# Performance work log

Measured on AMD Instinct MI355X. Metric: run time of the kernel, lower is better.

The kernel has to match this reference:

```python
import jax, jax.numpy as jnp
from jax import lax
import numpy as np

D_MODEL = 768
D_STATE = 64
D_CONV = 4
EXPAND = 2
D_INNER = EXPAND * D_MODEL          # 1536
HEADDIM = 64
H = D_INNER // HEADDIM              # 24 heads
CONV_DIM = D_INNER + 2 * D_STATE    # 1664 (x, B, C share the conv)
D_IN_PROJ = 2 * D_INNER + 2 * D_STATE + H  # z, xBC, dt
BATCH, SEQ = 4, 4096


def _mamba2(x, in_w, conv_w, conv_b, dt_bias, A_log, Dp, norm_w, out_w):
    """Mamba2 forward (ngroups=1, no in/out-proj bias), faithful to mamba_ssm reference path."""
    Bb, L, _ = x.shape
    zxbcdt = x @ in_w.T                                   # (B,L,D_IN_PROJ)
    z = zxbcdt[..., :D_INNER]
    xBC = zxbcdt[..., D_INNER:D_INNER + CONV_DIM]
    dt = zxbcdt[..., D_INNER + CONV_DIM:]                 # (B,L,H)
    # causal depthwise conv1d over time + SiLU
    xBC = xBC.transpose(0, 2, 1)                          # (B,C,L)
    xBC = lax.conv_general_dilated(xBC, conv_w, (1,), [(D_CONV - 1, 0)],
                                   feature_group_count=CONV_DIM,
                                   dimension_numbers=('NCH', 'OIH', 'NCH'))
    xBC = jax.nn.silu(xBC + conv_b[None, :, None]).transpose(0, 2, 1)
    xs = xBC[..., :D_INNER].reshape(Bb, L, H, HEADDIM)    # (B,L,H,P)
    Bc = xBC[..., D_INNER:D_INNER + D_STATE]              # (B,L,N)
    Cc = xBC[..., D_INNER + D_STATE:]                     # (B,L,N)
    dt = jax.nn.softplus(dt + dt_bias)                    # (B,L,H)
    dA = jnp.exp(dt * (-jnp.exp(A_log)))                  # (B,L,H)
    dtx = dt[..., None] * xs                              # (B,L,H,P)

    def step(h, inp):
        dA_t, dtx_t, B_t, C_t = inp
        h = h * dA_t[:, :, None, None] + jnp.einsum('bhp,bn->bhpn', dtx_t, B_t)
        y = jnp.einsum('bhpn,bn->bhp', h, C_t)
        return h, y

    h0 = jnp.zeros((Bb, H, HEADDIM, D_STATE), x.dtype)
    _, ys = lax.scan(step, h0, (jnp.moveaxis(dA, 1, 0), jnp.moveaxis(dtx, 1, 0),
                                jnp.moveaxis(Bc, 1, 0), jnp.moveaxis(Cc, 1, 0)))
    y = jnp.moveaxis(ys, 0, 1) + Dp[None, None, :, None] * xs  # skip term D*x
    y = y.reshape(Bb, L, D_INNER)
    # RMSNormGated (norm_before_gate=False): gate then normalize
    y = y * jax.nn.silu(z)
    y = y * lax.rsqrt(jnp.mean(y * y, -1, keepdims=True) + 1e-5) * norm_w
    return y @ out_w.T                                    # (B,L,D_MODEL)


def _mamba_params(key, scale=0.02):
    ks = jax.random.split(key, 5)
    in_w = jax.random.normal(ks[0], (D_IN_PROJ, D_MODEL), jnp.float32) * scale
    conv_w = jax.random.normal(ks[1], (CONV_DIM, 1, D_CONV), jnp.float32) * 0.2
    conv_b = jnp.zeros((CONV_DIM,), jnp.float32)
    dt = jax.random.uniform(ks[2], (H,), jnp.float32, 0.001, 0.1)
    dt_bias = dt + jnp.log(-jnp.expm1(-dt))               # inverse softplus
    A_log = jnp.log(jax.random.uniform(ks[3], (H,), jnp.float32, 1.0, 16.0))
    Dp = jnp.ones((H,), jnp.float32)
    norm_w = jnp.ones((D_INNER,), jnp.float32)
    out_w = jax.random.normal(ks[4], (D_MODEL, D_INNER), jnp.float32) * scale
    return in_w, conv_w, conv_b, dt_bias, A_log, Dp, norm_w, out_w


def setup_inputs() -> dict:
    key = jax.random.key(0)
    kx, kf, kb, kw = jax.random.split(key, 4)
    x = jax.random.normal(kx, (BATCH, SEQ, D_MODEL), jnp.float32)
    f = _mamba_params(kf)
    b = _mamba_params(kb)
    fus_w = jax.random.normal(kw, (D_MODEL, 2 * D_MODEL), jnp.float32) * 0.02
    fus_b = jnp.zeros((D_MODEL,), jnp.float32)
    names = ['in_w', 'conv_w', 'conv_b', 'dt_bias', 'A_log', 'D', 'norm_w', 'out_w']
    inp = {'x': x, 'fus_w': fus_w, 'fus_b': fus_b}
    for n, v in zip(names, f):
        inp['f_' + n] = v
    for n, v in zip(names, b):
        inp['b_' + n] = v
    return inp


def reference(x, fus_w, fus_b,
              f_in_w, f_conv_w, f_conv_b, f_dt_bias, f_A_log, f_D, f_norm_w, f_out_w,
              b_in_w, b_conv_w, b_conv_b, b_dt_bias, b_A_log, b_D, b_norm_w, b_out_w):
    out_f = _mamba2(x, f_in_w, f_conv_w, f_conv_b, f_dt_bias, f_A_log, f_D, f_norm_w, f_out_w)
    out_b = jnp.flip(_mamba2(jnp.flip(x, 1), b_in_w, b_conv_w, b_conv_b,
                             b_dt_bias, b_A_log, b_D, b_norm_w, b_out_w), 1)
    out = jnp.concatenate([out_f, out_b], axis=-1)        # (B,L,2*D_MODEL)
    return out @ fus_w.T + fus_b
```

## Files before the change

kernel.cpp:

```cpp
#include <hip/hip_runtime.h>
#include <hip/hip_bf16.h>


#define BATCHN 4
#define SEQL 4096
#define DMODEL 768
#define DINNER 1536
#define DSTATE 64
#define HN 24
#define CONVDIM 1664
#define NROWS_XBC 3200
#define NTOK (BATCHN*SEQL)
#define NCHUNK 64
#define LS 72

typedef short v8s __attribute__((ext_vector_type(8)));
typedef unsigned short v8u __attribute__((ext_vector_type(8)));
typedef float v4f __attribute__((ext_vector_type(4)));
typedef unsigned int v2u32 __attribute__((ext_vector_type(2)));
typedef __hip_bfloat16 bf16;

__device__ __forceinline__ int flip_row(int r) {
  return (r & ~4095) | (4095 - (r & 4095));
}
__device__ __forceinline__ float us2f(unsigned short u) {
  return __uint_as_float(((unsigned int)u) << 16);
}
__device__ __forceinline__ unsigned short f2us(float f) {
  bf16 b = __float2bfloat16(f);
  return __builtin_bit_cast(unsigned short, b);
}
__device__ __forceinline__ void async16(const unsigned short* g, unsigned short* l) {
  __builtin_amdgcn_global_load_lds(
      (const __attribute__((address_space(1))) unsigned int*)(const void*)g,
      (__attribute__((address_space(3))) unsigned int*)(void*)l, 16, 0, 0);
}


__global__ void cast_x_kernel(const float* __restrict__ x, bf16* __restrict__ xf) {
  int idx = blockIdx.x * 256 + threadIdx.x;
  v4f v = *(const v4f*)(x + (size_t)idx * 4);
  v2u32 o;
  o[0] = (unsigned int)f2us(v[0]) | ((unsigned int)f2us(v[1]) << 16);
  o[1] = (unsigned int)f2us(v[2]) | ((unsigned int)f2us(v[3]) << 16);
  *(v2u32*)((unsigned short*)xf + (size_t)idx * 4) = o;
}

__global__ void cast_kernel(const float* __restrict__ src, bf16* __restrict__ dst) {
  int idx = blockIdx.x * 256 + threadIdx.x;
  v4f v = *(const v4f*)(src + (size_t)idx * 4);
  v2u32 o;
  o[0] = (unsigned int)f2us(v[0]) | ((unsigned int)f2us(v[1]) << 16);
  o[1] = (unsigned int)f2us(v[2]) | ((unsigned int)f2us(v[3]) << 16);
  *(v2u32*)((unsigned short*)dst + (size_t)idx * 4) = o;
}

__global__ void cast_strided_kernel(const float* __restrict__ src, bf16* __restrict__ dst,
                                    int cols, int src_stride) {
  int idx4 = (blockIdx.x * 256 + threadIdx.x) * 4;
  int j = idx4 / cols, m = idx4 % cols;
  v4f v = *(const v4f*)(src + (size_t)j * src_stride + m);
  v2u32 o;
  o[0] = (unsigned int)f2us(v[0]) | ((unsigned int)f2us(v[1]) << 16);
  o[1] = (unsigned int)f2us(v[2]) | ((unsigned int)f2us(v[3]) << 16);
  *(v2u32*)((unsigned short*)dst + idx4) = o;
}

__global__ void transpose_ow_kernel(const float* __restrict__ src, bf16* __restrict__ dst) {
  int idx4 = (blockIdx.x * 256 + threadIdx.x) * 4;
  int k = idx4 / DMODEL, c0 = idx4 % DMODEL;
  unsigned short u[4];
#pragma unroll
  for (int i = 0; i < 4; i++)
    u[i] = f2us(src[(size_t)(c0 + i) * DINNER + k]);
  v2u32 o;
  o[0] = (unsigned int)u[0] | ((unsigned int)u[1] << 16);
  o[1] = (unsigned int)u[2] | ((unsigned int)u[3] << 16);
  *(v2u32*)((unsigned short*)dst + idx4) = o;
}

template <bool OUT_BF16>
__global__ __launch_bounds__(256) void gemm_lds(
    const bf16* __restrict__ A, const bf16* __restrict__ B, void* __restrict__ C,
    int K, int ldc, int flip_a, int flip_c, int accum, const float* __restrict__ bias) {
  __shared__ unsigned short sA[128 * 32];
  __shared__ unsigned short sB[128 * 32];
  int tid = threadIdx.x;
  int wave = tid >> 6, lane = tid & 63;
  int l15 = lane & 15, quad = lane >> 4;
  int m0 = blockIdx.x * 128, n0 = blockIdx.y * 128;
  int mw = (wave >> 1) * 64, nw = (wave & 1) * 64;

  int srow = wave * 32 + (lane >> 2);
  int scol = (lane & 3) * 8;
  const unsigned short* Ap = (const unsigned short*)A;
  const unsigned short* Bp = (const unsigned short*)B;
  int ar0 = m0 + srow, ar1 = m0 + srow + 16;
  if (flip_a) { ar0 = flip_row(ar0); ar1 = flip_row(ar1); }
  const unsigned short* ga0 = Ap + (size_t)ar0 * K + scol;
  const unsigned short* ga1 = Ap + (size_t)ar1 * K + scol;
  const unsigned short* gb0 = Bp + (size_t)(n0 + srow) * K + scol;
  const unsigned short* gb1 = Bp + (size_t)(n0 + srow + 16) * K + scol;
  unsigned short* lA0 = &sA[(wave * 32) * 32];
  unsigned short* lA1 = &sA[(wave * 32 + 16) * 32];
  unsigned short* lB0 = &sB[(wave * 32) * 32];
  unsigned short* lB1 = &sB[(wave * 32 + 16) * 32];

  v4f acc[4][4];
#pragma unroll
  for (int i = 0; i < 4; i++)
#pragma unroll
    for (int j = 0; j < 4; j++) acc[i][j] = {0.f, 0.f, 0.f, 0.f};

  for (int k0 = 0; k0 < K; k0 += 32) {
    async16(ga0 + k0, lA0);
    async16(ga1 + k0, lA1);
    async16(gb0 + k0, lB0);
    async16(gb1 + k0, lB1);
    __syncthreads();
    v8s af[4], bfr[4];
#pragma unroll
    for (int i = 0; i < 4; i++)
      af[i] = *(const v8s*)&sA[(mw + i * 16 + l15) * 32 + quad * 8];
#pragma unroll
    for (int j = 0; j < 4; j++)
      bfr[j] = *(const v8s*)&sB[(nw + j * 16 + l15) * 32 + quad * 8];
#pragma unroll
    for (int i = 0; i < 4; i++)
#pragma unroll
      for (int j = 0; j < 4; j++)
        acc[i][j] = __builtin_amdgcn_mfma_f32_16x16x32_bf16(af[i], bfr[j], acc[i][j], 0, 0, 0);
    __syncthreads();
  }

  float bv[4];
#pragma unroll
  for (int j = 0; j < 4; j++) bv[j] = bias ? bias[n0 + nw + j * 16 + l15] : 0.f;

#pragma unroll
  for (int i = 0; i < 4; i++) {
#pragma unroll
    for (int r = 0; r < 4; r++) {
      int row = m0 + mw + i * 16 + quad * 4 + r;
      int orow = flip_c ? flip_row(row) : row;
#pragma unroll
      for (int j = 0; j < 4; j++) {
        int col = n0 + nw + j * 16 + l15;
        float v = acc[i][j][r] + bv[j];
        size_t off = (size_t)orow * ldc + col;
        if (OUT_BF16) {
          ((bf16*)C)[off] = __float2bfloat16(v);
        } else {
          float* Cf = (float*)C;
          if (accum) v += Cf[off];
          Cf[off] = v;
        }
      }
    }
  }
}

__global__ __launch_bounds__(256) void dt_fused_kernel(
    const float* __restrict__ x,
    const float* __restrict__ in_w0, const float* __restrict__ in_w1,
    const float* __restrict__ dt_bias0, const float* __restrict__ dt_bias1,
    const float* __restrict__ A_log0, const float* __restrict__ A_log1,
    float* __restrict__ dt0, float* __restrict__ dl0,
    float* __restrict__ dt1, float* __restrict__ dl1) {
  __shared__ float sXT[64][128];
  __shared__ float sW[24][64];
  int tid = threadIdx.x;
  int tok2 = tid & 63, cg = tid >> 6;
  int dir = blockIdx.y;
  int tok_base = blockIdx.x * 128;

  int st_tok = tid >> 1, st_k0 = (tid & 1) * 32;
  const float* xg = x + (size_t)(tok_base + st_tok) * DMODEL + st_k0;
  const float* wb = dir ? in_w1 : in_w0;
  const float* wrow = wb + (size_t)NROWS_XBC * DMODEL;

  float acc0[6], acc1[6];
#pragma unroll
  for (int c = 0; c < 6; c++) { acc0[c] = 0.f; acc1[c] = 0.f; }

#pragma unroll 1
  for (int kc = 0; kc < 12; kc++) {
#pragma unroll
    for (int i = 0; i < 8; i++) {
      v4f v = *(const v4f*)(xg + kc * 64 + i * 4);
#pragma unroll
      for (int j = 0; j < 4; j++) sXT[st_k0 + i * 4 + j][st_tok] = v[j];
    }
    for (int i = tid; i < 24 * 16; i += 256) {
      int col = i >> 4, k4 = i & 15;
      *(v4f*)&sW[col][k4 * 4] =
          *(const v4f*)(wrow + (size_t)col * DMODEL + kc * 64 + k4 * 4);
    }
    __syncthreads();
#pragma unroll 2
    for (int k4 = 0; k4 < 16; k4++) {
      float xa[4], xb[4];
#pragma unroll
      for (int j = 0; j < 4; j++) {
        xa[j] = sXT[k4 * 4 + j][tok2];
        xb[j] = sXT[k4 * 4 + j][tok2 + 64];
      }
#pragma unroll
      for (int c = 0; c < 6; c++) {
        v4f wv = *(const v4f*)&sW[cg * 6 + c][k4 * 4];
#pragma unroll
        for (int j = 0; j < 4; j++) {
          acc0[c] = fmaf(xa[j], wv[j], acc0[c]);
          acc1[c] = fmaf(xb[j], wv[j], acc1[c]);
        }
      }
    }
    __syncthreads();
  }

  const float* dtB = dir ? dt_bias1 : dt_bias0;
  const float* Alg = dir ? A_log1 : A_log0;
  float* dto = dir ? dt1 : dt0;
  float* dlo = dir ? dl1 : dl0;
#pragma unroll
  for (int t = 0; t < 2; t++) {
    int r = tok_base + t * 64 + tok2;
    size_t row = dir ? (size_t)flip_row(r) : (size_t)r;
#pragma unroll
    for (int c = 0; c < 6; c++) {
      int h = cg * 6 + c;
      float v = (t ? acc1[c] : acc0[c]) + dtB[h];
      float dtv = (v > 20.f) ? v : log1pf(expf(v));
      dto[row * HN + h] = dtv;
      dlo[row * HN + h] = -dtv * expf(Alg[h]);
    }
  }
}

__global__ void conv_bc_kernel(const bf16* __restrict__ xbcr,
                               const float* __restrict__ conv_w,
                               const float* __restrict__ conv_b,
                               bf16* __restrict__ Bblob, bf16* __restrict__ Cblob) {
  int idx = blockIdx.x * 256 + threadIdx.x;
  int token = idx >> 4, oct = idx & 15;
  int b = token >> 12, l = token & 4095, c = l >> 6, s = l & 63;
  int ch0 = 1536 + oct * 8;
  const unsigned short* xp = (const unsigned short*)xbcr;
  v8u tv[4];
#pragma unroll
  for (int j = 0; j < 4; j++) {
    int ls = l - 3 + j;
    v8u z = {0, 0, 0, 0, 0, 0, 0, 0};
    tv[j] = z;
    if (ls >= 0)
      tv[j] = *(const v8u*)(xp + (size_t)((b << 12) | ls) * CONVDIM + ch0);
  }
  v8u ov;
#pragma unroll
  for (int e = 0; e < 8; e++) {
    int ch = ch0 + e;
    const float* w4 = conv_w + ch * 4;
    float acc = conv_b[ch];
#pragma unroll
    for (int j = 0; j < 4; j++) acc += us2f(tv[j][e]) * w4[j];
    ov[e] = f2us(acc / (1.f + __expf(-acc)));
  }
  size_t base = ((size_t)((b * 64 + c) * 64 + s)) * 64;
  int ch7 = oct * 8;
  if (ch7 < 64) *(v8u*)((unsigned short*)Bblob + base + ch7) = ov;
  else          *(v8u*)((unsigned short*)Cblob + base + ch7 - 64) = ov;
}

__global__ __launch_bounds__(256) void chunk_intra_kernel(
    const bf16* __restrict__ xbcr, const bf16* __restrict__ Bblob,
    const bf16* __restrict__ Cblob, const float* __restrict__ conv_w,
    const float* __restrict__ conv_b, const float* __restrict__ dtb,
    const float* __restrict__ dlb, const float* __restrict__ Dp,
    bf16* __restrict__ Yblob, bf16* __restrict__ Gblob, float* __restrict__ laq) {
  int blk = blockIdx.x;
  int c = blk & 63, bh = blk >> 6;
  int h = bh % HN, b = bh / HN;
  int tid = threadIdx.x, lane = tid & 63, wv = tid >> 6;
  int l15 = lane & 15, quad = lane >> 4;
  int tok0 = b * SEQL + c * 64;

  __shared__ unsigned short sXT[64][LS];
  __shared__ unsigned short sB [64][LS];
  __shared__ unsigned short sBT[64][LS];
  __shared__ unsigned short sC [64][LS];
  __shared__ union { unsigned short rawX[67][72]; unsigned short W[64][LS]; } sU;
  __shared__ float sla[64], sdt[64], sdG[64];

  for (int i = tid; i < 536; i += 256) {
    int r = i >> 3, j = i & 7;
    int l = c * 64 + r - 3;
    v8u v = {0, 0, 0, 0, 0, 0, 0, 0};
    if (l >= 0)
      v = *(const v8u*)((const unsigned short*)xbcr +
                        (size_t)(b * SEQL + l) * CONVDIM + h * 64 + j * 8);
    *(v8u*)&sU.rawX[r][j * 8] = v;
  }
  {
    const v8u* gB = (const v8u*)((const unsigned short*)Bblob + ((size_t)(b * 64 + c)) * 4096);
    const v8u* gC = (const v8u*)((const unsigned short*)Cblob + ((size_t)(b * 64 + c)) * 4096);
    int r0 = tid >> 3, g0 = tid & 7;
#pragma unroll
    for (int it = 0; it < 2; it++) {
      int row = r0 + it * 32;
      *(v8u*)&sB[row][g0 * 8] = gB[row * 8 + g0];
      *(v8u*)&sC[row][g0 * 8] = gC[row * 8 + g0];
    }
  }
  if (wv == 0) {
    float dtv = dtb[(size_t)(tok0 + lane) * HN + h];
    float lg = dlb[(size_t)(tok0 + lane) * HN + h];
#pragma unroll
    for (int d = 1; d < 64; d <<= 1) {
      float o = __shfl_up(lg, d);
      if (lane >= d) lg += o;
    }
    sla[lane] = lg;
    sdt[lane] = dtv;
    float la63 = __shfl(lg, 63);
    sdG[lane] = __expf(la63 - lg) * dtv;
    if (lane == 63) laq[blk] = __expf(la63);
  }
  __syncthreads();

  float Dh = Dp[h];
  {
    int s = lane;
#pragma unroll
    for (int o = 0; o < 2; o++) {
      int p0 = (wv * 2 + o) * 8;
      v8u r0 = *(const v8u*)&sU.rawX[s + 0][p0];
      v8u r1 = *(const v8u*)&sU.rawX[s + 1][p0];
      v8u r2 = *(const v8u*)&sU.rawX[s + 2][p0];
      v8u r3 = *(const v8u*)&sU.rawX[s + 3][p0];
#pragma unroll
      for (int pp = 0; pp < 8; pp++) {
        int ch = h * 64 + p0 + pp;
        const float* w4 = conv_w + ch * 4;
        float acc = conv_b[ch] + us2f(r0[pp]) * w4[0] + us2f(r1[pp]) * w4[1] +
                    us2f(r2[pp]) * w4[2] + us2f(r3[pp]) * w4[3];
        sXT[p0 + pp][s] = f2us(acc / (1.f + __expf(-acc)));
      }
    }
#pragma unroll
    for (int it = 0; it < 16; it++) {
      int n = wv + it * 4;
      sBT[n][s] = f2us(us2f(sB[s][n]) * sdG[s]);
    }
  }
  __syncthreads();

  {
    v4f acc[4];
#pragma unroll
    for (int j = 0; j < 4; j++) acc[j] = {0.f, 0.f, 0.f, 0.f};
    __builtin_amdgcn_s_setprio(1);
#pragma unroll
    for (int k0 = 0; k0 < 2; k0++) {
      v8s a = *(const v8s*)&sC[16 * wv + l15][k0 * 32 + quad * 8];
#pragma unroll
      for (int j = 0; j < 4; j++) {
        v8s bb = *(const v8s*)&sB[16 * j + l15][k0 * 32 + quad * 8];
        acc[j] = __builtin_amdgcn_mfma_f32_16x16x32_bf16(a, bb, acc[j], 0, 0, 0);
      }
    }
    __builtin_amdgcn_s_setprio(0);
    float lat[4];
#pragma unroll
    for (int r = 0; r < 4; r++) lat[r] = sla[16 * wv + quad * 4 + r];
#pragma unroll
    for (int j = 0; j < 4; j++) {
      int s = 16 * j + l15;
      float las = sla[s], dts = sdt[s];
#pragma unroll
      for (int r = 0; r < 4; r++) {
        int t = 16 * wv + quad * 4 + r;
        float w = (s <= t) ? __expf(lat[r] - las) * dts * acc[j][r] : 0.f;
        sU.W[t][s] = f2us(w);
      }
    }
  }
  __syncthreads();

  {
    v4f ya[4], ga[4];
#pragma unroll
    for (int j = 0; j < 4; j++) {
      ya[j] = {0.f, 0.f, 0.f, 0.f};
      ga[j] = {0.f, 0.f, 0.f, 0.f};
    }
    __builtin_amdgcn_s_setprio(1);
#pragma unroll
    for (int k0 = 0; k0 < 2; k0++) {
      v8s aw = *(const v8s*)&sU.W[16 * wv + l15][k0 * 32 + quad * 8];
      v8s ax = *(const v8s*)&sXT[16 * wv + l15][k0 * 32 + quad * 8];
#pragma unroll
      for (int j = 0; j < 4; j++) {
        v8s bx = *(const v8s*)&sXT[16 * j + l15][k0 * 32 + quad * 8];
        v8s bt = *(const v8s*)&sBT[16 * j + l15][k0 * 32 + quad * 8];
        ya[j] = __builtin_amdgcn_mfma_f32_16x16x32_bf16(aw, bx, ya[j], 0, 0, 0);
        ga[j] = __builtin_amdgcn_mfma_f32_16x16x32_bf16(ax, bt, ga[j], 0, 0, 0);
      }
    }
    __builtin_amdgcn_s_setprio(0);
#pragma unroll
    for (int j = 0; j < 4; j++) {
      int col = 16 * j + l15;
#pragma unroll
      for (int r = 0; r < 4; r++) {
        int row = 16 * wv + quad * 4 + r;
        float yv = ya[j][r] + Dh * us2f(sXT[col][row]);
        sB[row][col] = f2us(yv);
        sC[row][col] = f2us(ga[j][r]);
      }
    }
  }
  __syncthreads();

  {
    v8u* gY = (v8u*)(Yblob + (size_t)blk * 4096);
    v8u* gG = (v8u*)(Gblob + (size_t)blk * 4096);
#pragma unroll
    for (int it = 0; it < 2; it++) {
      int i = tid + it * 256;
      int row = i >> 3, j = i & 7;
      gY[row * 8 + j] = *(const v8u*)&sB[row][j * 8];
      gG[row * 8 + j] = *(const v8u*)&sC[row][j * 8];
    }
  }
}

__global__ __launch_bounds__(256) void state_scan_kernel(
    bf16* __restrict__ blob, const float* __restrict__ laq) {
  int bh = blockIdx.x;
  int tid = threadIdx.x;
  size_t base = (size_t)bh * 64 * 4096 + (size_t)(tid >> 2) * 64 + (size_t)(tid & 3) * 16;
  float S[16];
#pragma unroll
  for (int i = 0; i < 16; i++) S[i] = 0.f;
  for (int c = 0; c < 64; c++) {
    float q = laq[bh * 64 + c];
    unsigned short* gp = (unsigned short*)blob + base + (size_t)c * 4096;
    v8u ga = ((v8u*)gp)[0], gb = ((v8u*)gp)[1];
    v8u pa, pb;
#pragma unroll
    for (int i = 0; i < 8; i++) {
      pa[i] = f2us(S[i]);
      pb[i] = f2us(S[8 + i]);
    }
    ((v8u*)gp)[0] = pa;
    ((v8u*)gp)[1] = pb;
#pragma unroll
    for (int i = 0; i < 8; i++) {
      S[i] = q * S[i] + us2f(ga[i]);
      S[8 + i] = q * S[8 + i] + us2f(gb[i]);
    }
  }
}

__global__ __launch_bounds__(256) void chunk_inter_kernel(
    const bf16* __restrict__ Cblob, const float* __restrict__ dlb,
    const bf16* __restrict__ blob, bf16* __restrict__ Yblob) {
  int blk = blockIdx.x;
  int c = blk & 63, bh = blk >> 6;
  int h = bh % HN, b = bh / HN;
  int tid = threadIdx.x, lane = tid & 63, wv = tid >> 6;
  int l15 = lane & 15, quad = lane >> 4;
  int tok0 = b * SEQL + c * 64;

  __shared__ unsigned short sC[64][LS];
  __shared__ unsigned short sY[64][LS];
  __shared__ float sel[64];

  {
    const v8u* gC = (const v8u*)((const unsigned short*)Cblob + ((size_t)(b * 64 + c)) * 4096);
    int r0 = tid >> 3, g0 = tid & 7;
#pragma unroll
    for (int it = 0; it < 2; it++) {
      int row = r0 + it * 32;
      *(v8u*)&sC[row][g0 * 8] = gC[row * 8 + g0];
    }
  }
  if (wv == 0) {
    float lg = dlb[(size_t)(tok0 + lane) * HN + h];
#pragma unroll
    for (int d = 1; d < 64; d <<= 1) {
      float o = __shfl_up(lg, d);
      if (lane >= d) lg += o;
    }
    sel[lane] = __expf(lg);
  }
  __syncthreads();
  {
    v4f acc[4];
#pragma unroll
    for (int j = 0; j < 4; j++) acc[j] = {0.f, 0.f, 0.f, 0.f};
    const unsigned short* gS = (const unsigned short*)blob + (size_t)blk * 4096;
    __builtin_amdgcn_s_setprio(1);
#pragma unroll
    for (int k0 = 0; k0 < 2; k0++) {
      v8s a = *(const v8s*)&sC[16 * wv + l15][k0 * 32 + quad * 8];
#pragma unroll
      for (int j = 0; j < 4; j++) {
        v8s bS = *(const v8s*)(gS + (size_t)(16 * j + l15) * 64 + k0 * 32 + quad * 8);
        acc[j] = __builtin_amdgcn_mfma_f32_16x16x32_bf16(a, bS, acc[j], 0, 0, 0);
      }
    }
    __builtin_amdgcn_s_setprio(0);
    float selt[4];
#pragma unroll
    for (int r = 0; r < 4; r++) selt[r] = sel[16 * wv + quad * 4 + r];
#pragma unroll
    for (int j = 0; j < 4; j++)
#pragma unroll
      for (int r = 0; r < 4; r++)
        sY[16 * wv + quad * 4 + r][16 * j + l15] = f2us(selt[r] * acc[j][r]);
  }
  __syncthreads();
  {
    v8u* gY = (v8u*)(Yblob + (size_t)blk * 4096);
#pragma unroll
    for (int it = 0; it < 2; it++) {
      int i = tid + it * 256;
      int row = i >> 3, j = i & 7;
      v8u old = gY[row * 8 + j];
      v8u add = *(const v8u*)&sY[row][j * 8];
      v8u outv;
#pragma unroll
      for (int e = 0; e < 8; e++) outv[e] = f2us(us2f(old[e]) + us2f(add[e]));
      gY[row * 8 + j] = outv;
    }
  }
}

__global__ __launch_bounds__(256) void norm_kernel(
    const bf16* __restrict__ Yblob, const bf16* __restrict__ z,
    const float* __restrict__ norm_w, bf16* __restrict__ out) {
  int token = blockIdx.x;
  int tid = threadIdx.x;
  int b = token >> 12, l = token & 4095, c = l >> 6, t = l & 63;
  const unsigned short* zp = (const unsigned short*)z + (size_t)token * DINNER;
  float vals[6];
  float ss = 0.f;
#pragma unroll
  for (int i = 0; i < 3; i++) {
    int q = tid + i * 256;
    int ch = q * 2;
    int hh = ch >> 6, p = ch & 63;
    size_t yi = ((((size_t)(b * HN + hh)) * 64 + c) * 64 + t) * 64 + p;
    unsigned int yv2 = *(const unsigned int*)((const unsigned short*)Yblob + yi);
    unsigned int zv2 = *(const unsigned int*)(zp + ch);
#pragma unroll
    for (int e = 0; e < 2; e++) {
      float yv = us2f((unsigned short)((yv2 >> (16 * e)) & 0xffff));
      float zv = us2f((unsigned short)((zv2 >> (16 * e)) & 0xffff));
      float g = zv / (1.f + __expf(-zv));
      float v = yv * g;
      vals[i * 2 + e] = v;
      ss += v * v;
    }
  }
  for (int off = 32; off > 0; off >>= 1) ss += __shfl_down(ss, off);
  __shared__ float sred[4];
  if ((tid & 63) == 0) sred[tid >> 6] = ss;
  __syncthreads();
  float tot = sred[0] + sred[1] + sred[2] + sred[3];
  float scale = rsqrtf(tot / (float)DINNER + 1e-5f);
#pragma unroll
  for (int i = 0; i < 3; i++) {
    int q = tid + i * 256;
    int ch = q * 2;
    unsigned int o =
        (unsigned int)f2us(vals[i * 2] * scale * norm_w[ch]) |
        ((unsigned int)f2us(vals[i * 2 + 1] * scale * norm_w[ch + 1]) << 16);
    *(unsigned int*)((unsigned short*)out + (size_t)token * DINNER + ch) = o;
  }
}

extern "C" void kernel_launch(void* const* d_in, const int* in_sizes, int n_in,
                              void* d_out, int out_size, void* d_ws, size_t ws_size,
                              hipStream_t stream) {
  const float* x = (const float*)d_in[0];
  const float* fus_w = (const float*)d_in[1];
  const float* fus_b = (const float*)d_in[2];
  const float* in_w[2] = {(const float*)d_in[3], (const float*)d_in[11]};
  const float* conv_w[2] = {(const float*)d_in[4], (const float*)d_in[12]};
  const float* conv_b[2] = {(const float*)d_in[5], (const float*)d_in[13]};
  const float* dt_bias[2] = {(const float*)d_in[6], (const float*)d_in[14]};
  const float* A_log[2] = {(const float*)d_in[7], (const float*)d_in[15]};
  const float* Dp[2] = {(const float*)d_in[8], (const float*)d_in[16]};
  const float* norm_w[2] = {(const float*)d_in[9], (const float*)d_in[17]};
  const float* out_w[2] = {(const float*)d_in[10], (const float*)d_in[18]};
  (void)in_sizes; (void)n_in;

  char* ws = (char*)d_ws;
  size_t off = 0;
  auto alloc = [&](size_t bytes) {
    size_t o = off;
    off = (off + bytes + 255) & ~(size_t)255;
    return o;
  };
  bf16* x_bf  = (bf16*)(ws + alloc((size_t)NTOK * DMODEL * 2));
  bf16* w_in  = (bf16*)(ws + alloc((size_t)NROWS_XBC * DMODEL * 2));
  bf16* wf1   = (bf16*)(ws + alloc((size_t)DMODEL * DMODEL * 2));
  bf16* owT   = (bf16*)(ws + alloc((size_t)DINNER * DMODEL * 2));
  bf16* wc    = (bf16*)(ws + alloc((size_t)DMODEL * DINNER * 2));
  bf16* xbcr  = (bf16*)(ws + alloc((size_t)NTOK * CONVDIM * 2));
  float* dtb0 = (float*)(ws + alloc((size_t)NTOK * HN * 4));
  float* dlb0 = (float*)(ws + alloc((size_t)NTOK * HN * 4));
  float* dtb1 = (float*)(ws + alloc((size_t)NTOK * HN * 4));
  float* dlb1 = (float*)(ws + alloc((size_t)NTOK * HN * 4));
  float* laq  = (float*)(ws + alloc((size_t)BATCHN * HN * NCHUNK * 4));
  bf16* Bblob = (bf16*)(ws + alloc((size_t)NTOK * DSTATE * 2));
  bf16* Cblob = (bf16*)(ws + alloc((size_t)NTOK * DSTATE * 2));
  bf16* Gblob = (bf16*)(ws + alloc((size_t)NTOK * DINNER * 2));
  bf16* Yblob = (bf16*)(ws + alloc((size_t)NTOK * DINNER * 2));
  bf16* zbuf  = Gblob;
  bf16* ynorm = xbcr;
  float* dtbs[2] = {dtb0, dtb1};
  float* dlbs[2] = {dlb0, dlb1};

  if (ws_size < off) {
    hipMemsetAsync(d_out, 0, (size_t)out_size * 4, stream);
    return;
  }

  cast_x_kernel<<<(NTOK * DMODEL) / 1024, 256, 0, stream>>>(x, x_bf);
  dt_fused_kernel<<<dim3(NTOK / 128, 2), 256, 0, stream>>>(
      x, in_w[0], in_w[1], dt_bias[0], dt_bias[1], A_log[0], A_log[1],
      dtb0, dlb0, dtb1, dlb1);

  for (int dir = 0; dir < 2; dir++) {
    cast_kernel<<<(NROWS_XBC * DMODEL) / 1024, 256, 0, stream>>>(in_w[dir], w_in);
    gemm_lds<true><<<dim3(NTOK / 128, CONVDIM / 128), 256, 0, stream>>>(
        x_bf, w_in + (size_t)DINNER * DMODEL, xbcr, DMODEL, CONVDIM, dir, 0, 0, nullptr);
    conv_bc_kernel<<<(NTOK * 16) / 256, 256, 0, stream>>>(
        xbcr, conv_w[dir], conv_b[dir], Bblob, Cblob);
    chunk_intra_kernel<<<BATCHN * HN * NCHUNK, 256, 0, stream>>>(
        xbcr, Bblob, Cblob, conv_w[dir], conv_b[dir], dtbs[dir], dlbs[dir], Dp[dir],
        Yblob, Gblob, laq);
    state_scan_kernel<<<BATCHN * HN, 256, 0, stream>>>(Gblob, laq);
    chunk_inter_kernel<<<BATCHN * HN * NCHUNK, 256, 0, stream>>>(Cblob, dlbs[dir], Gblob, Yblob);
    gemm_lds<true><<<dim3(NTOK / 128, DINNER / 128), 256, 0, stream>>>(
        x_bf, w_in, zbuf, DMODEL, DINNER, dir, 0, 0, nullptr);
    norm_kernel<<<NTOK, 256, 0, stream>>>(Yblob, zbuf, norm_w[dir], ynorm);
    cast_strided_kernel<<<(DMODEL * DMODEL) / 1024, 256, 0, stream>>>(
        fus_w + dir * DMODEL, wf1, DMODEL, 2 * DMODEL);
    transpose_ow_kernel<<<(DINNER * DMODEL) / 1024, 256, 0, stream>>>(out_w[dir], owT);
    gemm_lds<true><<<dim3(DMODEL / 128, DINNER / 128), 256, 0, stream>>>(
        wf1, owT, wc, DMODEL, DINNER, 0, 0, 0, nullptr);
    gemm_lds<false><<<dim3(NTOK / 128, DMODEL / 128), 256, 0, stream>>>(
        ynorm, wc, d_out, DINNER, DMODEL, 0, dir, dir, dir == 0 ? fus_b : nullptr);
  }
}
```

Baseline: 959.6 us.

## Double-buffer LDS tiles in GEMM and swizzle workgroups across XCDs

The bf16 MFMA GEMM now uses two LDS buffers per operand, so the async global-to-LDS load for the next K-slice is issued before the MFMAs on the current slice. This aims to hide global memory latency behind compute, and it leaves one barrier per iteration. Workgroup indices are also remapped so that consecutive tiles land on the same XCD, which should improve L2 reuse. LDS use doubles to 32 KB per block, which could lower occupancy. The loop's sync ordering looks correct only because the trailing __syncthreads is kept.

```diff
diff --git a/kernel.cpp b/kernel.cpp
--- a/kernel.cpp
+++ b/kernel.cpp
@@ -13,6 +13,7 @@
 #define NTOK (BATCHN*SEQL)
 #define NCHUNK 64
 #define LS 72
+#define GBUF (128 * 32)
 
 typedef short v8s __attribute__((ext_vector_type(8)));
 typedef unsigned short v8u __attribute__((ext_vector_type(8)));
@@ -83,12 +84,19 @@
 __global__ __launch_bounds__(256) void gemm_lds(
     const bf16* __restrict__ A, const bf16* __restrict__ B, void* __restrict__ C,
     int K, int ldc, int flip_a, int flip_c, int accum, const float* __restrict__ bias) {
-  __shared__ unsigned short sA[128 * 32];
-  __shared__ unsigned short sB[128 * 32];
+  __shared__ unsigned short sA[2 * GBUF];
+  __shared__ unsigned short sB[2 * GBUF];
   int tid = threadIdx.x;
   int wave = tid >> 6, lane = tid & 63;
   int l15 = lane & 15, quad = lane >> 4;
-  int m0 = blockIdx.x * 128, n0 = blockIdx.y * 128;
+
+  int gx = gridDim.x;
+  int nwg = gx * gridDim.y;
+  int lin = blockIdx.y * gx + blockIdx.x;
+  int q = nwg >> 3, r = nwg & 7;
+  int xcd = lin & 7, rank = lin >> 3;
+  int swz = (xcd < r ? xcd * (q + 1) : r * (q + 1) + (xcd - r) * q) + rank;
+  int m0 = (swz % gx) * 128, n0 = (swz / gx) * 128;
   int mw = (wave >> 1) * 64, nw = (wave & 1) * 64;
 
   int srow = wave * 32 + (lane >> 2);
@@ -101,10 +109,8 @@
   const unsigned short* ga1 = Ap + (size_t)ar1 * K + scol;
   const unsigned short* gb0 = Bp + (size_t)(n0 + srow) * K + scol;
   const unsigned short* gb1 = Bp + (size_t)(n0 + srow + 16) * K + scol;
-  unsigned short* lA0 = &sA[(wave * 32) * 32];
-  unsigned short* lA1 = &sA[(wave * 32 + 16) * 32];
-  unsigned short* lB0 = &sB[(wave * 32) * 32];
-  unsigned short* lB1 = &sB[(wave * 32 + 16) * 32];
+  int lo0 = (wave * 32) * 32;
+  int lo1 = (wave * 32 + 16) * 32;
 
   v4f acc[4][4];
 #pragma unroll
@@ -112,19 +118,30 @@
 #pragma unroll
     for (int j = 0; j < 4; j++) acc[i][j] = {0.f, 0.f, 0.f, 0.f};
 
-  for (int k0 = 0; k0 < K; k0 += 32) {
-    async16(ga0 + k0, lA0);
-    async16(ga1 + k0, lA1);
-    async16(gb0 + k0, lB0);
-    async16(gb1 + k0, lB1);
-    __syncthreads();
+  async16(ga0, &sA[lo0]);
+  async16(ga1, &sA[lo1]);
+  async16(gb0, &sB[lo0]);
+  async16(gb1, &sB[lo1]);
+  __syncthreads();
+
+  int nt = K >> 5;
+  for (int t = 0; t < nt; t++) {
+    int cur = (t & 1) * GBUF;
+    if (t + 1 < nt) {
+      int k0 = (t + 1) << 5;
+      int nx = ((t + 1) & 1) * GBUF;
+      async16(ga0 + k0, &sA[nx + lo0]);
+      async16(ga1 + k0, &sA[nx + lo1]);
+      async16(gb0 + k0, &sB[nx + lo0]);
+      async16(gb1 + k0, &sB[nx + lo1]);
+    }
     v8s af[4], bfr[4];
 #pragma unroll
     for (int i = 0; i < 4; i++)
-      af[i] = *(const v8s*)&sA[(mw + i * 16 + l15) * 32 + quad * 8];
+      af[i] = *(const v8s*)&sA[cur + (mw + i * 16 + l15) * 32 + quad * 8];
 #pragma unroll
     for (int j = 0; j < 4; j++)
-      bfr[j] = *(const v8s*)&sB[(nw + j * 16 + l15) * 32 + quad * 8];
+      bfr[j] = *(const v8s*)&sB[cur + (nw + j * 16 + l15) * 32 + quad * 8];
 #pragma unroll
     for (int i = 0; i < 4; i++)
 #pragma unroll
@@ -140,13 +157,13 @@
 #pragma unroll
   for (int i = 0; i < 4; i++) {
 #pragma unroll
-    for (int r = 0; r < 4; r++) {
-      int row = m0 + mw + i * 16 + quad * 4 + r;
+    for (int r2 = 0; r2 < 4; r2++) {
+      int row = m0 + mw + i * 16 + quad * 4 + r2;
       int orow = flip_c ? flip_row(row) : row;
 #pragma unroll
       for (int j = 0; j < 4; j++) {
         int col = n0 + nw + j * 16 + l15;
-        float v = acc[i][j][r] + bv[j];
+        float v = acc[i][j][r2] + bv[j];
         size_t off = (size_t)orow * ldc + col;
         if (OUT_BF16) {
           ((bf16*)C)[off] = __float2bfloat16(v);
```

Result: no change. 970.4 us (+1.1%).
